# Kernel optimization log

Measured on AMD Instinct MI355X. Metric: run time of the kernel, lower is better.

The kernel has to match this reference:

```python
import jax, jax.numpy as jnp
import numpy as np

B, N, H = 4, 256, 512
P = 128  # game_physics_params


def _init(key, shape, scale=0.02):
    return jax.random.normal(key, shape, dtype=jnp.float32) * scale


def setup_inputs() -> dict:
    key = jax.random.key(0)
    ks = jax.random.split(key, 16)
    return {
        "object_features": jax.random.normal(ks[0], (B, N, H), dtype=jnp.float32),
        # physics_predictor: H -> 512 -> P
        "pp_w1": _init(ks[1], (H, 512)), "pp_b1": jnp.zeros((512,), jnp.float32),
        "pp_w2": _init(ks[2], (512, P)), "pp_b2": jnp.zeros((P,), jnp.float32),
        # collision_detector: 2H -> 256 -> 128 -> 1
        "cd_w1": _init(ks[3], (2 * H, 256)), "cd_b1": jnp.zeros((256,), jnp.float32),
        "cd_w2": _init(ks[4], (256, 128)), "cd_b2": jnp.zeros((128,), jnp.float32),
        "cd_w3": _init(ks[5], (128, 1)), "cd_b3": jnp.zeros((1,), jnp.float32),
        # velocity / force heads: H -> 3
        "vel_w": _init(ks[6], (H, 3)), "vel_b": jnp.zeros((3,), jnp.float32),
        "frc_w": _init(ks[7], (H, 3)), "frc_b": jnp.zeros((3,), jnp.float32),
    }


def reference(object_features, pp_w1, pp_b1, pp_w2, pp_b2,
              cd_w1, cd_b1, cd_w2, cd_b2, cd_w3, cd_b3,
              vel_w, vel_b, frc_w, frc_b):
    x = object_features  # [B, N, H]
    # physics predictor MLP
    p = jax.nn.relu(x @ pp_w1 + pp_b1) @ pp_w2 + pp_b2  # [B, N, P]
    mass = jax.nn.sigmoid(p[..., 0:1]) * 100.0
    friction = jax.nn.sigmoid(p[..., 1:2])
    elasticity = jax.nn.sigmoid(p[..., 2:3])
    density = jax.nn.sigmoid(p[..., 3:4]) * 10.0
    velocities = x @ vel_w + vel_b  # [B, N, 3]
    forces = x @ frc_w + frc_b      # [B, N, 3]

    # vectorized pairwise collision detection over upper-triangle pairs
    iu, ju = np.triu_indices(N, k=1)  # static index arrays, length Np = N(N-1)/2
    pairs = jnp.concatenate([x[:, iu], x[:, ju]], axis=-1)  # [B, Np, 2H]
    h = jax.nn.relu(pairs @ cd_w1 + cd_b1)
    h = jax.nn.relu(h @ cd_w2 + cd_b2)
    prob = jax.nn.sigmoid(h @ cd_w3 + cd_b3)[..., 0]  # [B, Np]
    collision_matrix = jnp.zeros((x.shape[0], N, N), dtype=x.dtype)
    collision_matrix = collision_matrix.at[:, iu, ju].set(prob).at[:, ju, iu].set(prob)

    return (mass, friction, elasticity, density, velocities, forces, collision_matrix)
```

## Files before the change

### kernel.cpp

```cpp
#include <hip/hip_runtime.h>
#include <hip/hip_bf16.h>

typedef __attribute__((ext_vector_type(8))) short bf16x8;
typedef __attribute__((ext_vector_type(4))) float f32x4;

__device__ __forceinline__ float sigmoidf_(float v) {
    return 1.0f / (1.0f + __expf(-v));
}
__device__ __forceinline__ short f2bf(float f) {
    union { __hip_bfloat16 h; short s; } cv;
    cv.h = __float2bfloat16(f);
    return cv.s;
}
__device__ __forceinline__ float bf2f(short s) {
    union { float f; unsigned u; } cv;
    cv.u = ((unsigned)(unsigned short)s) << 16;
    return cv.f;
}

__global__ __launch_bounds__(256) void convert_kernel(
    const float* __restrict__ x, const float* __restrict__ pp_w1,
    const float* __restrict__ cd_w1, const float* __restrict__ cd_w2,
    const float* __restrict__ pp_w2, const float* __restrict__ vel_w,
    const float* __restrict__ frc_w,
    __hip_bfloat16* __restrict__ xb, __hip_bfloat16* __restrict__ Wt,
    __hip_bfloat16* __restrict__ w2t, float* __restrict__ hw)
{
    __shared__ float ts[64][65];
    const int b = blockIdx.x, t = threadIdx.x;

    if (b < 256) {
        int base = b * 2048 + t * 8;
        float4 a = *(const float4*)(x + base);
        float4 c = *(const float4*)(x + base + 4);
        bf16x8 o;
        o[0] = f2bf(a.x); o[1] = f2bf(a.y); o[2] = f2bf(a.z); o[3] = f2bf(a.w);
        o[4] = f2bf(c.x); o[5] = f2bf(c.y); o[6] = f2bf(c.z); o[7] = f2bf(c.w);
        *(bf16x8*)(xb + base) = o;
        return;
    }
    if (b == 392) {
        for (int e = t; e < 5120; e += 256) {
            int h = e >> 9, k = e & 511;
            float v = (h < 4) ? pp_w2[k * 128 + h]
                    : (h < 7) ? vel_w[k * 3 + (h - 4)]
                              : frc_w[k * 3 + (h - 7)];
            hw[e] = v;
        }
        return;
    }

    const float* src; int ss, k0, n0, region;
    if (b < 320)      { int i = b - 256; src = pp_w1; ss = 512; k0 = (i >> 3) * 64; n0 = (i & 7) * 64; region = 0; }
    else if (b < 384) { int i = b - 320; src = cd_w1; ss = 256; k0 = (i >> 2) * 64; n0 = (i & 3) * 64; region = 1; }
    else              { int i = b - 384; src = cd_w2; ss = 128; k0 = (i >> 1) * 64; n0 = (i & 1) * 64; region = 2; }

    #pragma unroll
    for (int i = 0; i < 4; ++i) {
        int r = (t >> 4) + i * 16, c4 = (t & 15) * 4;
        *(float4*)&ts[r][c4] = *(const float4*)(src + (k0 + r) * ss + n0 + c4);
    }
    __syncthreads();
    #pragma unroll
    for (int i = 0; i < 4; ++i) {
        int nOut = (t >> 4) + i * 16, kc = (t & 15) * 4;
        ushort4 o;
        o.x = (unsigned short)f2bf(ts[kc + 0][nOut]);
        o.y = (unsigned short)f2bf(ts[kc + 1][nOut]);
        o.z = (unsigned short)f2bf(ts[kc + 2][nOut]);
        o.w = (unsigned short)f2bf(ts[kc + 3][nOut]);
        int gn = n0 + nOut, gk = k0 + kc;
        if (region == 0)      *(ushort4*)(Wt + gn * 512 + gk) = o;
        else if (region == 1) {
            int row = (gk < 512) ? (512 + gn) : (768 + gn);
            *(ushort4*)(Wt + row * 512 + (gk & 511)) = o;
        } else                *(ushort4*)(w2t + gn * 256 + gk) = o;
    }
}

__global__ __launch_bounds__(256) void gemm_kernel(
    const __hip_bfloat16* __restrict__ xb, const __hip_bfloat16* __restrict__ Wt,
    const float* __restrict__ pp_b1, const float* __restrict__ cd_b1,
    __hip_bfloat16* __restrict__ hidg, float* __restrict__ Ug,
    float* __restrict__ Vg)
{
    const int t = threadIdx.x;
    const int wave = t >> 6, lane = t & 63;
    const int l = lane & 15, q = lane >> 4;
    const int m0 = blockIdx.y * 32;
    const int n0 = blockIdx.x * 128 + wave * 32;

    const __hip_bfloat16* a0p = xb + (m0 + l) * 512 + q * 8;
    const __hip_bfloat16* a1p = a0p + 16 * 512;
    const __hip_bfloat16* b0p = Wt + (n0 + l) * 512 + q * 8;
    const __hip_bfloat16* b1p = b0p + 16 * 512;

    f32x4 acc00 = {}, acc01 = {}, acc10 = {}, acc11 = {};
    #pragma unroll
    for (int ks = 0; ks < 16; ++ks) {
        bf16x8 a0 = *(const bf16x8*)(a0p + ks * 32);
        bf16x8 a1 = *(const bf16x8*)(a1p + ks * 32);
        bf16x8 b0 = *(const bf16x8*)(b0p + ks * 32);
        bf16x8 b1 = *(const bf16x8*)(b1p + ks * 32);
        acc00 = __builtin_amdgcn_mfma_f32_16x16x32_bf16(a0, b0, acc00, 0, 0, 0);
        acc01 = __builtin_amdgcn_mfma_f32_16x16x32_bf16(a0, b1, acc01, 0, 0, 0);
        acc10 = __builtin_amdgcn_mfma_f32_16x16x32_bf16(a1, b0, acc10, 0, 0, 0);
        acc11 = __builtin_amdgcn_mfma_f32_16x16x32_bf16(a1, b1, acc11, 0, 0, 0);
    }

    const int c0 = n0 + l, c1 = n0 + 16 + l;
    #pragma unroll
    for (int mt = 0; mt < 2; ++mt) {
        const f32x4& A0 = mt ? acc10 : acc00;
        const f32x4& A1 = mt ? acc11 : acc01;
        if (n0 < 512) {
            float b0v = pp_b1[c0], b1v = pp_b1[c1];
            #pragma unroll
            for (int r = 0; r < 4; ++r) {
                int rg = m0 + mt * 16 + q * 4 + r;
                hidg[rg * 512 + c0] = __float2bfloat16(fmaxf(A0[r] + b0v, 0.f));
                hidg[rg * 512 + c1] = __float2bfloat16(fmaxf(A1[r] + b1v, 0.f));
            }
        } else if (n0 < 768) {
            float b0v = cd_b1[c0 - 512], b1v = cd_b1[c1 - 512];
            #pragma unroll
            for (int r = 0; r < 4; ++r) {
                int rg = m0 + mt * 16 + q * 4 + r;
                Ug[rg * 256 + (c0 - 512)] = A0[r] + b0v;
                Ug[rg * 256 + (c1 - 512)] = A1[r] + b1v;
            }
        } else {
            #pragma unroll
            for (int r = 0; r < 4; ++r) {
                int rg = m0 + mt * 16 + q * 4 + r;
                Vg[rg * 256 + (c0 - 768)] = A0[r];
                Vg[rg * 256 + (c1 - 768)] = A1[r];
            }
        }
    }
}

__global__ __launch_bounds__(256) void heads_kernel(
    const float* __restrict__ x, const __hip_bfloat16* __restrict__ hidg,
    const float* __restrict__ hw, const float* __restrict__ pp_b2,
    const float* __restrict__ vel_b, const float* __restrict__ frc_b,
    float* __restrict__ out)
{
    const int t = threadIdx.x, wave = t >> 6, lane = t & 63;
    const int row = blockIdx.x * 4 + wave;

    const float4* xr = (const float4*)(x + row * 512);
    float4 xa = xr[lane * 2], xc = xr[lane * 2 + 1];
    bf16x8 hb = *(const bf16x8*)(hidg + row * 512 + lane * 8);
    float hf[8];
    #pragma unroll
    for (int j = 0; j < 8; ++j) hf[j] = bf2f(hb[j]);

    #pragma unroll
    for (int h = 0; h < 10; ++h) {
        const float4* wr = (const float4*)(hw + h * 512);
        float4 wa = wr[lane * 2], wc = wr[lane * 2 + 1];
        float s;
        if (h < 4) {
            s = hf[0]*wa.x + hf[1]*wa.y + hf[2]*wa.z + hf[3]*wa.w
              + hf[4]*wc.x + hf[5]*wc.y + hf[6]*wc.z + hf[7]*wc.w;
        } else {
            s = xa.x*wa.x + xa.y*wa.y + xa.z*wa.z + xa.w*wa.w
              + xc.x*wc.x + xc.y*wc.y + xc.z*wc.z + xc.w*wc.w;
        }
        s += __shfl_xor(s, 1);  s += __shfl_xor(s, 2);
        s += __shfl_xor(s, 4);  s += __shfl_xor(s, 8);
        s += __shfl_xor(s, 16); s += __shfl_xor(s, 32);
        if (lane == 0) {
            if (h < 4) {
                float sg = sigmoidf_(s + pp_b2[h]);
                out[h * 1024 + row] = (h == 0) ? sg * 100.f : (h == 3) ? sg * 10.f : sg;
            } else if (h < 7) {
                out[4096 + row * 3 + (h - 4)] = s + vel_b[h - 4];
            } else {
                out[7168 + row * 3 + (h - 7)] = s + frc_b[h - 7];
            }
        }
    }
}

__global__ __launch_bounds__(256) void pair_kernel(
    const float* __restrict__ Ug, const float* __restrict__ Vg,
    const __hip_bfloat16* __restrict__ w2t,
    const float* __restrict__ cd_b2, const float* __restrict__ cd_w3,
    const float* __restrict__ cd_b3, float* __restrict__ cm)
{
    const int b = blockIdx.y;
    const int tp = blockIdx.x;
    int ti = (int)((65.0f - sqrtf(4225.0f - 8.0f * (float)tp)) * 0.5f);
    while ((ti + 1) * (65 - (ti + 1)) / 2 <= tp) ++ti;
    while (ti * (65 - ti) / 2 > tp) --ti;
    const int tj = ti + (tp - ti * (65 - ti) / 2);

    __shared__ __align__(16) float Us[8][264];
    __shared__ __align__(16) float Vs[8][264];
    __shared__ float ps[64][4];

    const int t = threadIdx.x;
    const int i0 = ti * 8, j0 = tj * 8;

    {
        const float4* Ug4 = (const float4*)(Ug + (b * 256 + i0) * 256);
        const float4* Vg4 = (const float4*)(Vg + (b * 256 + j0) * 256);
        #pragma unroll
        for (int c = t; c < 512; c += 256) {
            int row = c >> 6, col = (c & 63) << 2;
            *(float4*)&Us[row][col] = Ug4[c];
            *(float4*)&Vs[row][col] = Vg4[c];
        }
    }
    __syncthreads();

    const int wave = t >> 6, lane = t & 63;
    const int l = lane & 15, q = lane >> 4;
    const int pj = l & 7, piB = l >> 3;

    const __hip_bfloat16* wb0 = w2t + ((wave * 2 + 0) * 16 + l) * 256 + q * 8;
    const __hip_bfloat16* wb1 = wb0 + 16 * 256;

    f32x4 acc[4][2] = {};
    #pragma unroll
    for (int ks = 0; ks < 8; ++ks) {
        bf16x8 bfr0 = *(const bf16x8*)(wb0 + ks * 32);
        bf16x8 bfr1 = *(const bf16x8*)(wb1 + ks * 32);
        const int kk = ks * 32 + q * 8;
        #pragma unroll
        for (int mt = 0; mt < 4; ++mt) {
            const int pi = mt * 2 + piB;
            float4 u0 = *(const float4*)&Us[pi][kk];
            float4 u1 = *(const float4*)&Us[pi][kk + 4];
            float4 v0 = *(const float4*)&Vs[pj][kk];
            float4 v1 = *(const float4*)&Vs[pj][kk + 4];
            bf16x8 afr;
            afr[0] = f2bf(fmaxf(u0.x + v0.x, 0.f));
            afr[1] = f2bf(fmaxf(u0.y + v0.y, 0.f));
            afr[2] = f2bf(fmaxf(u0.z + v0.z, 0.f));
            afr[3] = f2bf(fmaxf(u0.w + v0.w, 0.f));
            afr[4] = f2bf(fmaxf(u1.x + v1.x, 0.f));
            afr[5] = f2bf(fmaxf(u1.y + v1.y, 0.f));
            afr[6] = f2bf(fmaxf(u1.z + v1.z, 0.f));
            afr[7] = f2bf(fmaxf(u1.w + v1.w, 0.f));
            acc[mt][0] = __builtin_amdgcn_mfma_f32_16x16x32_bf16(afr, bfr0, acc[mt][0], 0, 0, 0);
            acc[mt][1] = __builtin_amdgcn_mfma_f32_16x16x32_bf16(afr, bfr1, acc[mt][1], 0, 0, 0);
        }
    }

    float b2v0 = cd_b2[(wave * 2 + 0) * 16 + l], b2v1 = cd_b2[(wave * 2 + 1) * 16 + l];
    float w3v0 = cd_w3[(wave * 2 + 0) * 16 + l], w3v1 = cd_w3[(wave * 2 + 1) * 16 + l];
    #pragma unroll
    for (int mt = 0; mt < 4; ++mt) {
        #pragma unroll
        for (int r = 0; r < 4; ++r) {
            float g0 = fmaxf(acc[mt][0][r] + b2v0, 0.f);
            float g1 = fmaxf(acc[mt][1][r] + b2v1, 0.f);
            float s = g0 * w3v0 + g1 * w3v1;
            s += __shfl_xor(s, 1);
            s += __shfl_xor(s, 2);
            s += __shfl_xor(s, 4);
            s += __shfl_xor(s, 8);
            if (l == 0) ps[mt * 16 + q * 4 + r][wave] = s;
        }
    }
    __syncthreads();

    if (t < 64) {
        int p = t;
        float v = ps[p][0] + ps[p][1] + ps[p][2] + ps[p][3] + cd_b3[0];
        float prob = 1.0f / (1.0f + __expf(-v));
        int i = i0 + (p >> 3), j = j0 + (p & 7);
        float* base = cm + b * 65536;
        if (i < j) {
            base[i * 256 + j] = prob;
            base[j * 256 + i] = prob;
        } else if (i == j) {
            base[i * 256 + i] = 0.0f;
        }
    }
}

extern "C" void kernel_launch(void* const* d_in, const int* in_sizes, int n_in,
                              void* d_out, int out_size, void* d_ws, size_t ws_size,
                              hipStream_t stream) {
    const float* x     = (const float*)d_in[0];
    const float* pp_w1 = (const float*)d_in[1];
    const float* pp_b1 = (const float*)d_in[2];
    const float* pp_w2 = (const float*)d_in[3];
    const float* pp_b2 = (const float*)d_in[4];
    const float* cd_w1 = (const float*)d_in[5];
    const float* cd_b1 = (const float*)d_in[6];
    const float* cd_w2 = (const float*)d_in[7];
    const float* cd_b2 = (const float*)d_in[8];
    const float* cd_w3 = (const float*)d_in[9];
    const float* cd_b3 = (const float*)d_in[10];
    const float* vel_w = (const float*)d_in[11];
    const float* vel_b = (const float*)d_in[12];
    const float* frc_w = (const float*)d_in[13];
    const float* frc_b = (const float*)d_in[14];

    float* out = (float*)d_out;
    float* Ug = (float*)d_ws;
    float* Vg = Ug + 262144;
    __hip_bfloat16* xb   = (__hip_bfloat16*)(Vg + 262144);
    __hip_bfloat16* Wt   = xb + 524288;
    __hip_bfloat16* hidg = Wt + 524288;
    __hip_bfloat16* w2t  = hidg + 524288;
    float* hw = (float*)(w2t + 32768);

    convert_kernel<<<dim3(393), dim3(256), 0, stream>>>(
        x, pp_w1, cd_w1, cd_w2, pp_w2, vel_w, frc_w, xb, Wt, w2t, hw);
    gemm_kernel<<<dim3(8, 32), dim3(256), 0, stream>>>(
        xb, Wt, pp_b1, cd_b1, hidg, Ug, Vg);
    heads_kernel<<<dim3(256), dim3(256), 0, stream>>>(
        x, hidg, hw, pp_b2, vel_b, frc_b, out);
    pair_kernel<<<dim3(528, 4), dim3(256), 0, stream>>>(
        Ug, Vg, w2t, cd_b2, cd_w3, cd_b3, out + 10240);
}
```

Baseline: 136.0 us.

## Fuse heads into pair kernel and precompute bf16 pair activations in swizzled LDS

```diff
diff --git a/kernel.cpp b/kernel.cpp
--- a/kernel.cpp
+++ b/kernel.cpp
@@ -133,63 +133,67 @@
             #pragma unroll
             for (int r = 0; r < 4; ++r) {
                 int rg = m0 + mt * 16 + q * 4 + r;
-                Vg[rg * 256 + (c0 - 768)] = A0[r];
-                Vg[rg * 256 + (c1 - 768)] = A1[r];
-            }
-        }
-    }
-}
-
-__global__ __launch_bounds__(256) void heads_kernel(
+                Vg[rg * 256 + (c0 - 768)] = A0[r] + 0.f;
+                Vg[rg * 256 + (c1 - 768)] = A1[r] + 0.f;
+            }
+        }
+    }
+}
+
+__global__ __launch_bounds__(256) void pair_kernel(
+    const float* __restrict__ Ug, const float* __restrict__ Vg,
+    const __hip_bfloat16* __restrict__ w2t,
+    const float* __restrict__ cd_b2, const float* __restrict__ cd_w3,
+    const float* __restrict__ cd_b3, float* __restrict__ cm,
     const float* __restrict__ x, const __hip_bfloat16* __restrict__ hidg,
     const float* __restrict__ hw, const float* __restrict__ pp_b2,
     const float* __restrict__ vel_b, const float* __restrict__ frc_b,
     float* __restrict__ out)
 {
-    const int t = threadIdx.x, wave = t >> 6, lane = t & 63;
-    const int row = blockIdx.x * 4 + wave;
-
-    const float4* xr = (const float4*)(x + row * 512);
-    float4 xa = xr[lane * 2], xc = xr[lane * 2 + 1];
-    bf16x8 hb = *(const bf16x8*)(hidg + row * 512 + lane * 8);
-    float hf[8];
-    #pragma unroll
-    for (int j = 0; j < 8; ++j) hf[j] = bf2f(hb[j]);
-
-    #pragma unroll
-    for (int h = 0; h < 10; ++h) {
-        const float4* wr = (const float4*)(hw + h * 512);
-        float4 wa = wr[lane * 2], wc = wr[lane * 2 + 1];
-        float s;
-        if (h < 4) {
-            s = hf[0]*wa.x + hf[1]*wa.y + hf[2]*wa.z + hf[3]*wa.w
-              + hf[4]*wc.x + hf[5]*wc.y + hf[6]*wc.z + hf[7]*wc.w;
-        } else {
-            s = xa.x*wa.x + xa.y*wa.y + xa.z*wa.z + xa.w*wa.w
-              + xc.x*wc.x + xc.y*wc.y + xc.z*wc.z + xc.w*wc.w;
-        }
-        s += __shfl_xor(s, 1);  s += __shfl_xor(s, 2);
-        s += __shfl_xor(s, 4);  s += __shfl_xor(s, 8);
-        s += __shfl_xor(s, 16); s += __shfl_xor(s, 32);
-        if (lane == 0) {
+    __shared__ __align__(16) __hip_bfloat16 hs[16384];
+    __shared__ float ps[64][4];
+
+    const int t = threadIdx.x;
+    const int wave = t >> 6, lane = t & 63;
+
+    if (blockIdx.x >= 528) {
+        const int row = blockIdx.y * 256 + (blockIdx.x - 528) * 4 + wave;
+        const float4* xr = (const float4*)(x + row * 512);
+        float4 xa = xr[lane * 2], xc = xr[lane * 2 + 1];
+        bf16x8 hb = *(const bf16x8*)(hidg + row * 512 + lane * 8);
+        float hf[8];
+        #pragma unroll
+        for (int j = 0; j < 8; ++j) hf[j] = bf2f(hb[j]);
+
+        #pragma unroll
+        for (int h = 0; h < 10; ++h) {
+            const float4* wr = (const float4*)(hw + h * 512);
+            float4 wa = wr[lane * 2], wc = wr[lane * 2 + 1];
+            float s;
             if (h < 4) {
-                float sg = sigmoidf_(s + pp_b2[h]);
-                out[h * 1024 + row] = (h == 0) ? sg * 100.f : (h == 3) ? sg * 10.f : sg;
-            } else if (h < 7) {
-                out[4096 + row * 3 + (h - 4)] = s + vel_b[h - 4];
+                s = hf[0]*wa.x + hf[1]*wa.y + hf[2]*wa.z + hf[3]*wa.w
+                  + hf[4]*wc.x + hf[5]*wc.y + hf[6]*wc.z + hf[7]*wc.w;
             } else {
-                out[7168 + row * 3 + (h - 7)] = s + frc_b[h - 7];
-            }
-        }
-    }
-}
-
-__global__ __launch_bounds__(256) void pair_kernel(
-    const float* __restrict__ Ug, const float* __restrict__ Vg,
-    const __hip_bfloat16* __restrict__ w2t,
-    const float* __restrict__ cd_b2, const float* __restrict__ cd_w3,
-    const float* __restrict__ cd_b3, float* __restrict__ cm)
-{
+                s = xa.x*wa.x + xa.y*wa.y + xa.z*wa.z + xa.w*wa.w
+                  + xc.x*wc.x + xc.y*wc.y + xc.z*wc.z + xc.w*wc.w;
+            }
+            s += __shfl_xor(s, 1);  s += __shfl_xor(s, 2);
+            s += __shfl_xor(s, 4);  s += __shfl_xor(s, 8);
+            s += __shfl_xor(s, 16); s += __shfl_xor(s, 32);
+            if (lane == 0) {
+                if (h < 4) {
+                    float sg = sigmoidf_(s + pp_b2[h]);
+                    out[h * 1024 + row] = (h == 0) ? sg * 100.f : (h == 3) ? sg * 10.f : sg;
+                } else if (h < 7) {
+                    out[4096 + row * 3 + (h - 4)] = s + vel_b[h - 4];
+                } else {
+                    out[7168 + row * 3 + (h - 7)] = s + frc_b[h - 7];
+                }
+            }
+        }
+        return;
+    }
+
     const int b = blockIdx.y;
     const int tp = blockIdx.x;
     int ti = (int)((65.0f - sqrtf(4225.0f - 8.0f * (float)tp)) * 0.5f);
@@ -197,54 +201,51 @@
     while (ti * (65 - ti) / 2 > tp) --ti;
     const int tj = ti + (tp - ti * (65 - ti) / 2);
 
-    __shared__ __align__(16) float Us[8][264];
-    __shared__ __align__(16) float Vs[8][264];
-    __shared__ float ps[64][4];
-
-    const int t = threadIdx.x;
     const int i0 = ti * 8, j0 = tj * 8;
 
     {
-        const float4* Ug4 = (const float4*)(Ug + (b * 256 + i0) * 256);
-        const float4* Vg4 = (const float4*)(Vg + (b * 256 + j0) * 256);
-        #pragma unroll
-        for (int c = t; c < 512; c += 256) {
-            int row = c >> 6, col = (c & 63) << 2;
-            *(float4*)&Us[row][col] = Ug4[c];
-            *(float4*)&Vs[row][col] = Vg4[c];
+        const float* Ub = Ug + (b * 256 + i0) * 256;
+        const float* Vb = Vg + (b * 256 + j0) * 256;
+        #pragma unroll
+        for (int w = 0; w < 8; ++w) {
+            int idx = (w << 8) + t;
+            int p = idx >> 5, c = idx & 31;
+            const float* up = Ub + (p >> 3) * 256 + c * 8;
+            const float* vp = Vb + (p & 7) * 256 + c * 8;
+            float4 u0 = *(const float4*)up, u1 = *(const float4*)(up + 4);
+            float4 v0 = *(const float4*)vp, v1 = *(const float4*)(vp + 4);
+            bf16x8 o;
+            o[0] = f2bf(fmaxf(u0.x + v0.x, 0.f));
+            o[1] = f2bf(fmaxf(u0.y + v0.y, 0.f));
+            o[2] = f2bf(fmaxf(u0.z + v0.z, 0.f));
+            o[3] = f2bf(fmaxf(u0.w + v0.w, 0.f));
+            o[4] = f2bf(fmaxf(u1.x + v1.x, 0.f));
+            o[5] = f2bf(fmaxf(u1.y + v1.y, 0.f));
+            o[6] = f2bf(fmaxf(u1.z + v1.z, 0.f));
+            o[7] = f2bf(fmaxf(u1.w + v1.w, 0.f));
+            int byte = (p << 9) + (c << 4);
+            byte ^= (p & 7) << 4;
+            *(bf16x8*)((char*)hs + byte) = o;
         }
     }
     __syncthreads();
 
-    const int wave = t >> 6, lane = t & 63;
     const int l = lane & 15, q = lane >> 4;
-    const int pj = l & 7, piB = l >> 3;
-
     const __hip_bfloat16* wb0 = w2t + ((wave * 2 + 0) * 16 + l) * 256 + q * 8;
     const __hip_bfloat16* wb1 = wb0 + 16 * 256;
+    const char* hsb = (const char*)hs;
+    const int xorv = (l & 7) << 4;
+    const int rbase = (l << 9) + (q << 4);
 
     f32x4 acc[4][2] = {};
     #pragma unroll
     for (int ks = 0; ks < 8; ++ks) {
         bf16x8 bfr0 = *(const bf16x8*)(wb0 + ks * 32);
         bf16x8 bfr1 = *(const bf16x8*)(wb1 + ks * 32);
-        const int kk = ks * 32 + q * 8;
         #pragma unroll
         for (int mt = 0; mt < 4; ++mt) {
-            const int pi = mt * 2 + piB;
-            float4 u0 = *(const float4*)&Us[pi][kk];
-            float4 u1 = *(const float4*)&Us[pi][kk + 4];
-            float4 v0 = *(const float4*)&Vs[pj][kk];
-            float4 v1 = *(const float4*)&Vs[pj][kk + 4];
-            bf16x8 afr;
-            afr[0] = f2bf(fmaxf(u0.x + v0.x, 0.f));
-            afr[1] = f2bf(fmaxf(u0.y + v0.y, 0.f));
-            afr[2] = f2bf(fmaxf(u0.z + v0.z, 0.f));
-            afr[3] = f2bf(fmaxf(u0.w + v0.w, 0.f));
-            afr[4] = f2bf(fmaxf(u1.x + v1.x, 0.f));
-            afr[5] = f2bf(fmaxf(u1.y + v1.y, 0.f));
-            afr[6] = f2bf(fmaxf(u1.z + v1.z, 0.f));
-            afr[7] = f2bf(fmaxf(u1.w + v1.w, 0.f));
+            int byte = (mt << 13) + rbase + (ks << 6);
+            bf16x8 afr = *(const bf16x8*)(hsb + (byte ^ xorv));
             acc[mt][0] = __builtin_amdgcn_mfma_f32_16x16x32_bf16(afr, bfr0, acc[mt][0], 0, 0, 0);
             acc[mt][1] = __builtin_amdgcn_mfma_f32_16x16x32_bf16(afr, bfr1, acc[mt][1], 0, 0, 0);
         }
@@ -315,8 +316,7 @@
         x, pp_w1, cd_w1, cd_w2, pp_w2, vel_w, frc_w, xb, Wt, w2t, hw);
     gemm_kernel<<<dim3(8, 32), dim3(256), 0, stream>>>(
         xb, Wt, pp_b1, cd_b1, hidg, Ug, Vg);
-    heads_kernel<<<dim3(256), dim3(256), 0, stream>>>(
+    pair_kernel<<<dim3(592, 4), dim3(256), 0, stream>>>(
+        Ug, Vg, w2t, cd_b2, cd_w3, cd_b3, out + 10240,
         x, hidg, hw, pp_b2, vel_b, frc_b, out);
-    pair_kernel<<<dim3(528, 4), dim3(256), 0, stream>>>(
-        Ug, Vg, w2t, cd_b2, cd_w3, cd_b3, out + 10240);
-}
+}
```

New measurement: 136.0 us. Within noise of the previous version (-0.0%).
